# Kernel tuning notes

Measured on AMD Instinct MI355X. Metric: run time of the kernel, lower is better.

The kernel has to match this reference:

```python
import jax, jax.numpy as jnp
import numpy as np

EPS = 0.5
MIN_PTS = 10


def setup_inputs() -> dict:
    key = jax.random.key(0)
    point_features = jax.random.normal(key, (4, 8192, 16), dtype=jnp.float32)
    return {"point_features": point_features}


def reference(point_features) -> jnp.ndarray:
    # torch.cdist(x, x): pairwise Euclidean distances, shape [B, N, N]
    x = point_features
    sq = jnp.sum(x * x, axis=-1)                      # [B, N]
    # squared distances via ||a||^2 + ||b||^2 - 2 a.b
    d2 = sq[:, :, None] + sq[:, None, :] - 2.0 * jnp.einsum('bnd,bmd->bnm', x, x)
    dist = jnp.sqrt(jnp.maximum(d2, 0.0))             # [B, N, N]
    # neighbors = 1 where dist < eps (includes self, dist==0)
    neighbor_count = jnp.sum(dist < EPS, axis=2)      # [B, N] int
    # final_clusters starts at 0; points with too few neighbors marked -1 (noise)
    final_clusters = jnp.where(neighbor_count < MIN_PTS, -1, 0).astype(jnp.int32)
    return final_clusters
```

## Files before the change

### kernel.cpp

```cpp
#include <hip/hip_runtime.h>


constexpr int Np = 8192;
constexpr int Bb = 4;
constexpr int MIN_PTS = 10;
constexpr float EPS2_4 = 0.0625f;
constexpr int JS = 16;
constexpr int JW = Np / JS;
constexpr int ICH = 256;
constexpr int RF = 4;
constexpr int NT = JW / 16;

typedef __bf16 bf16x8 __attribute__((ext_vector_type(8)));
typedef float  f32x4  __attribute__((ext_vector_type(4)));

__global__ __launch_bounds__(256)
void dbscan_prep(const float* __restrict__ x, __bf16* __restrict__ aug,
                 int* __restrict__ out) {
    const int p = blockIdx.x * 256 + threadIdx.x;
    const float4* src = (const float4*)(x + (size_t)p * 16);
    float4 v0 = src[0], v1 = src[1], v2 = src[2], v3 = src[3];
    float vv[16];
    vv[0]=v0.x; vv[1]=v0.y; vv[2]=v0.z; vv[3]=v0.w;
    vv[4]=v1.x; vv[5]=v1.y; vv[6]=v1.z; vv[7]=v1.w;
    vv[8]=v2.x; vv[9]=v2.y; vv[10]=v2.z; vv[11]=v2.w;
    vv[12]=v3.x; vv[13]=v3.y; vv[14]=v3.z; vv[15]=v3.w;
    float s = 0.f;
#pragma unroll
    for (int k = 0; k < 16; k++) s = fmaf(vv[k], vv[k], s);
    const float g = 0.5f * s - EPS2_4;
    bf16x8 h0, h1, h2;
#pragma unroll
    for (int k = 0; k < 8; k++) { h0[k] = (__bf16)vv[k]; h1[k] = (__bf16)vv[k+8]; }
    h2[0] = (__bf16)1.0f; h2[1] = (__bf16)(-g);
#pragma unroll
    for (int k = 2; k < 8; k++) h2[k] = (__bf16)0.0f;
    bf16x8* dst = (bf16x8*)(aug + (size_t)p * 24);
    dst[0] = h0; dst[1] = h1; dst[2] = h2;
    out[p] = 0;
}

__global__ __launch_bounds__(256, 6)
void dbscan_count(const __bf16* __restrict__ aug, int* __restrict__ out) {
    const int lane = threadIdx.x & 63;
    const int w    = threadIdx.x >> 6;
    const int m    = lane & 15;
    const int q    = lane >> 4;
    const int blk  = blockIdx.x;
    const int b    = blk >> 9;
    const int ic   = (blk >> 4) & 31;
    const int js   = blk & 15;
    const size_t pbase = (size_t)b * Np;
    const int ibase = ic * ICH;
    const int jbase = js * JW;

    __shared__ __bf16 ldsB[NT * 48 * 8];

    {
        const __bf16* src = aug + (pbase + jbase) * 24;
#pragma unroll
        for (int it = 0; it < 6; it++) {
            const int c = threadIdx.x + it * 256;
            const int p = c / 3;
            const int r = c - p * 3;
            bf16x8 v = *(const bf16x8*)(src + (size_t)c * 8);
            *(bf16x8*)(ldsB + (((p >> 4) * 48) + r * 16 + (p & 15)) * 8) = v;
        }
    }

    bf16x8 af[RF];
#pragma unroll
    for (int f = 0; f < RF; f++) {
        const __bf16* ap = aug + (pbase + ibase + w * 64 + f * 16 + m) * 24 + q * 8;
        bf16x8 a = *(const bf16x8*)ap;
        if (q == 2) { __bf16 t = a[0]; a[0] = a[1]; a[1] = t; }
        if (q == 3) {
#pragma unroll
            for (int k = 0; k < 8; k++) a[k] = (__bf16)0.0f;
        }
        af[f] = a;
    }

    __syncthreads();

    const __bf16* bptr = ldsB + (q < 3 ? (q * 16 + m) * 8 : 0);

    const f32x4 zacc = {0.f, 0.f, 0.f, 0.f};
    int cnt[16];
#pragma unroll
    for (int i = 0; i < 16; i++) cnt[i] = 0;

    bf16x8 bc = *(const bf16x8*)bptr;
#pragma unroll 2
    for (int t = 0; t < NT; t++) {
        const int tn = (t + 1) & (NT - 1);
        bf16x8 bn = *(const bf16x8*)(bptr + tn * 48 * 8);
#pragma unroll
        for (int f = 0; f < RF; f++) {
            f32x4 acc = __builtin_amdgcn_mfma_f32_16x16x32_bf16(af[f], bc, zacc, 0, 0, 0);
            cnt[f*4+0] += __float_as_int(acc[0]) >> 31;
            cnt[f*4+1] += __float_as_int(acc[1]) >> 31;
            cnt[f*4+2] += __float_as_int(acc[2]) >> 31;
            cnt[f*4+3] += __float_as_int(acc[3]) >> 31;
        }
        bc = bn;
    }

#pragma unroll
    for (int i = 0; i < 16; i++) {
        int v = cnt[i];
        v += __shfl_xor(v, 1);
        v += __shfl_xor(v, 2);
        v += __shfl_xor(v, 4);
        v += __shfl_xor(v, 8);
        cnt[i] = v;
    }
    if (m == 0) {
        int* ob = out + pbase + ibase + w * 64;
#pragma unroll
        for (int f = 0; f < RF; f++)
#pragma unroll
            for (int r = 0; r < 4; r++)
                atomicAdd(&ob[f*16 + q*4 + r], JW + cnt[f*4+r]);
    }
}

__global__ __launch_bounds__(256)
void dbscan_classify(int* __restrict__ out) {
    const int p = blockIdx.x * 256 + threadIdx.x;
    out[p] = (out[p] < MIN_PTS) ? -1 : 0;
}

extern "C" void kernel_launch(void* const* d_in, const int* in_sizes, int n_in,
                              void* d_out, int out_size, void* d_ws, size_t ws_size,
                              hipStream_t stream) {
    const float* x = (const float*)d_in[0];
    int* out = (int*)d_out;
    __bf16* aug = (__bf16*)d_ws;

    dbscan_prep<<<dim3(Bb * Np / 256), dim3(256), 0, stream>>>(x, aug, out);
    dbscan_count<<<dim3(Bb * 32 * JS), dim3(256), 0, stream>>>(aug, out);
    dbscan_classify<<<dim3(Bb * Np / 256), dim3(256), 0, stream>>>(out);
}
```

Measured before the change: 76.02 us.

## Use 32x32x16 MFMA with fp32 norm bias in accumulator and ballot skip

```diff
diff --git a/kernel.cpp b/kernel.cpp
--- a/kernel.cpp
+++ b/kernel.cpp
@@ -8,15 +8,19 @@
 constexpr int JS = 16;
 constexpr int JW = Np / JS;
 constexpr int ICH = 256;
-constexpr int RF = 4;
-constexpr int NT = JW / 16;
+constexpr int NT = JW / 32;
 
 typedef __bf16 bf16x8 __attribute__((ext_vector_type(8)));
-typedef float  f32x4  __attribute__((ext_vector_type(4)));
+typedef float  f32x16 __attribute__((ext_vector_type(16)));
+
+#define GLOBAL_LOAD_LDS16(gptr, lptr)                                          \
+    __builtin_amdgcn_global_load_lds(                                          \
+        (const __attribute__((address_space(1))) void*)(gptr),                 \
+        (__attribute__((address_space(3))) void*)(lptr), 16, 0, 0)
 
 __global__ __launch_bounds__(256)
 void dbscan_prep(const float* __restrict__ x, __bf16* __restrict__ aug,
-                 int* __restrict__ out) {
+                 float* __restrict__ garr, int* __restrict__ out) {
     const int p = blockIdx.x * 256 + threadIdx.x;
     const float4* src = (const float4*)(x + (size_t)p * 16);
     float4 v0 = src[0], v1 = src[1], v2 = src[2], v3 = src[3];
@@ -28,100 +32,105 @@
     float s = 0.f;
 #pragma unroll
     for (int k = 0; k < 16; k++) s = fmaf(vv[k], vv[k], s);
-    const float g = 0.5f * s - EPS2_4;
-    bf16x8 h0, h1, h2;
+    bf16x8 h0, h1;
 #pragma unroll
     for (int k = 0; k < 8; k++) { h0[k] = (__bf16)vv[k]; h1[k] = (__bf16)vv[k+8]; }
-    h2[0] = (__bf16)1.0f; h2[1] = (__bf16)(-g);
-#pragma unroll
-    for (int k = 2; k < 8; k++) h2[k] = (__bf16)0.0f;
-    bf16x8* dst = (bf16x8*)(aug + (size_t)p * 24);
-    dst[0] = h0; dst[1] = h1; dst[2] = h2;
+    bf16x8* dst = (bf16x8*)(aug + (size_t)p * 16);
+    dst[0] = h0; dst[1] = h1;
+    garr[p] = 0.5f * s - EPS2_4;
     out[p] = 0;
 }
 
-__global__ __launch_bounds__(256, 6)
-void dbscan_count(const __bf16* __restrict__ aug, int* __restrict__ out) {
+__global__ __launch_bounds__(256, 4)
+void dbscan_count(const __bf16* __restrict__ aug, const float* __restrict__ garr,
+                  int* __restrict__ out) {
     const int lane = threadIdx.x & 63;
     const int w    = threadIdx.x >> 6;
-    const int m    = lane & 15;
-    const int q    = lane >> 4;
+    const int c31  = lane & 31;
+    const int h    = lane >> 5;
     const int blk  = blockIdx.x;
     const int b    = blk >> 9;
     const int ic   = (blk >> 4) & 31;
     const int js   = blk & 15;
-    const size_t pbase = (size_t)b * Np;
     const int ibase = ic * ICH;
     const int jbase = js * JW;
+    const size_t pb = (size_t)b * Np;
 
-    __shared__ __bf16 ldsB[NT * 48 * 8];
+    __shared__ __align__(16) __bf16 ldsW[JW * 16];
+    __shared__ __align__(16) float  ldsG[JW];
 
     {
-        const __bf16* src = aug + (pbase + jbase) * 24;
+        const __bf16* srcW = aug + (pb + jbase) * 16;
 #pragma unroll
-        for (int it = 0; it < 6; it++) {
+        for (int it = 0; it < 4; it++) {
             const int c = threadIdx.x + it * 256;
-            const int p = c / 3;
-            const int r = c - p * 3;
-            bf16x8 v = *(const bf16x8*)(src + (size_t)c * 8);
-            *(bf16x8*)(ldsB + (((p >> 4) * 48) + r * 16 + (p & 15)) * 8) = v;
+            GLOBAL_LOAD_LDS16(srcW + (size_t)c * 8, ldsW + (size_t)c * 8);
+        }
+        const float* srcG = garr + pb + jbase;
+        if (threadIdx.x < 128)
+            GLOBAL_LOAD_LDS16(srcG + threadIdx.x * 4, ldsG + threadIdx.x * 4);
+    }
+
+    const int rb = ibase + w * 64;
+    bf16x8 af[2];
+#pragma unroll
+    for (int f = 0; f < 2; f++)
+        af[f] = *(const bf16x8*)(aug + (pb + rb + f * 32 + c31) * 16 + h * 8);
+
+    float ngrow[2][16];
+#pragma unroll
+    for (int f = 0; f < 2; f++)
+#pragma unroll
+        for (int r = 0; r < 16; r++) {
+            const int row = (r & 3) + 8 * (r >> 2) + 4 * h;
+            ngrow[f][r] = -garr[pb + rb + f * 32 + row];
+        }
+
+    __syncthreads();
+
+    unsigned int cnt[16];
+#pragma unroll
+    for (int r = 0; r < 16; r++) cnt[r] = 0u;
+
+    for (int t = 0; t < NT; t++) {
+        const bf16x8 bc = *(const bf16x8*)(ldsW + ((t * 32 + c31) * 16 + h * 8));
+        const float  gc = ldsG[t * 32 + c31];
+#pragma unroll
+        for (int f = 0; f < 2; f++) {
+            f32x16 cin;
+#pragma unroll
+            for (int r = 0; r < 16; r++) cin[r] = ngrow[f][r] - gc;
+            f32x16 acc = __builtin_amdgcn_mfma_f32_32x32x16_bf16(af[f], bc, cin, 0, 0, 0);
+            float mx = acc[0];
+#pragma unroll
+            for (int r = 1; r < 16; r++) mx = fmaxf(mx, acc[r]);
+            if (__ballot(mx > 0.0f) != 0ull) {
+                const unsigned int step = f ? 0x10000u : 1u;
+#pragma unroll
+                for (int r = 0; r < 16; r++)
+                    cnt[r] += (acc[r] > 0.0f) ? step : 0u;
+            }
         }
     }
 
-    bf16x8 af[RF];
 #pragma unroll
-    for (int f = 0; f < RF; f++) {
-        const __bf16* ap = aug + (pbase + ibase + w * 64 + f * 16 + m) * 24 + q * 8;
-        bf16x8 a = *(const bf16x8*)ap;
-        if (q == 2) { __bf16 t = a[0]; a[0] = a[1]; a[1] = t; }
-        if (q == 3) {
-#pragma unroll
-            for (int k = 0; k < 8; k++) a[k] = (__bf16)0.0f;
-        }
-        af[f] = a;
-    }
-
-    __syncthreads();
-
-    const __bf16* bptr = ldsB + (q < 3 ? (q * 16 + m) * 8 : 0);
-
-    const f32x4 zacc = {0.f, 0.f, 0.f, 0.f};
-    int cnt[16];
-#pragma unroll
-    for (int i = 0; i < 16; i++) cnt[i] = 0;
-
-    bf16x8 bc = *(const bf16x8*)bptr;
-#pragma unroll 2
-    for (int t = 0; t < NT; t++) {
-        const int tn = (t + 1) & (NT - 1);
-        bf16x8 bn = *(const bf16x8*)(bptr + tn * 48 * 8);
-#pragma unroll
-        for (int f = 0; f < RF; f++) {
-            f32x4 acc = __builtin_amdgcn_mfma_f32_16x16x32_bf16(af[f], bc, zacc, 0, 0, 0);
-            cnt[f*4+0] += __float_as_int(acc[0]) >> 31;
-            cnt[f*4+1] += __float_as_int(acc[1]) >> 31;
-            cnt[f*4+2] += __float_as_int(acc[2]) >> 31;
-            cnt[f*4+3] += __float_as_int(acc[3]) >> 31;
-        }
-        bc = bn;
-    }
-
-#pragma unroll
-    for (int i = 0; i < 16; i++) {
-        int v = cnt[i];
+    for (int r = 0; r < 16; r++) {
+        unsigned int v = cnt[r];
         v += __shfl_xor(v, 1);
         v += __shfl_xor(v, 2);
         v += __shfl_xor(v, 4);
         v += __shfl_xor(v, 8);
-        cnt[i] = v;
+        v += __shfl_xor(v, 16);
+        cnt[r] = v;
     }
-    if (m == 0) {
-        int* ob = out + pbase + ibase + w * 64;
+    if (c31 == 0) {
+        int* ob = out + pb + rb;
 #pragma unroll
-        for (int f = 0; f < RF; f++)
-#pragma unroll
-            for (int r = 0; r < 4; r++)
-                atomicAdd(&ob[f*16 + q*4 + r], JW + cnt[f*4+r]);
+        for (int r = 0; r < 16; r++) {
+            const int row = (r & 3) + 8 * (r >> 2) + 4 * h;
+            atomicAdd(&ob[row],      (int)(cnt[r] & 0xffffu));
+            atomicAdd(&ob[32 + row], (int)(cnt[r] >> 16));
+        }
     }
 }
 
@@ -137,8 +146,9 @@
     const float* x = (const float*)d_in[0];
     int* out = (int*)d_out;
     __bf16* aug = (__bf16*)d_ws;
+    float* garr = (float*)((char*)d_ws + (1u << 20));
 
-    dbscan_prep<<<dim3(Bb * Np / 256), dim3(256), 0, stream>>>(x, aug, out);
-    dbscan_count<<<dim3(Bb * 32 * JS), dim3(256), 0, stream>>>(aug, out);
+    dbscan_prep<<<dim3(Bb * Np / 256), dim3(256), 0, stream>>>(x, aug, garr, out);
+    dbscan_count<<<dim3(Bb * 32 * JS), dim3(256), 0, stream>>>(aug, garr, out);
     dbscan_classify<<<dim3(Bb * Np / 256), dim3(256), 0, stream>>>(out);
 }
```

New measurement: 81.12 us. +6.7%, slower.
